# Kernel optimization log

Measured on AMD Instinct MI355X. Metric: run time of the kernel, lower is better.

## Reference

```python
import jax, jax.numpy as jnp
import numpy as np

SIGMA = 1.2
SIGMA_SQ = jnp.float32(SIGMA * SIGMA)


def setup_inputs() -> dict:
    key = jax.random.key(0)
    k1, k2, k3 = jax.random.split(key, 3)
    X = jax.random.normal(k1, (32768, 2), dtype=jnp.float32)
    pattern_layer = jax.random.normal(k2, (8192, 2), dtype=jnp.float32)
    W2 = jax.random.normal(k3, (8192,), dtype=jnp.float32)
    return {"X": X, "pattern_layer": pattern_layer, "W2": W2}


def reference(X, pattern_layer, W2):
    # Pairwise squared distances via |a|^2 + |b|^2 - 2 a.b  -> [N, P]
    x_sq = jnp.sum(X * X, axis=1, keepdims=True)              # [N, 1]
    p_sq = jnp.sum(pattern_layer * pattern_layer, axis=1)     # [P]
    cross = X @ pattern_layer.T                               # [N, P]
    Dsq = x_sq + p_sq[None, :] - 2.0 * cross                  # [N, P]
    K = jnp.exp(-Dsq / (2.0 * SIGMA_SQ))                      # RBF kernel [N, P]
    num = K @ W2                                              # [N]
    den = jnp.sum(K, axis=1)                                  # [N]
    return num / den
```

## Files before the change

kernel.cpp:

```cpp
#include <hip/hip_runtime.h>

#define N 32768
#define P 8192
#define SLICES 16
#define XPB 64
#define PATS_PER_SLICE (P / SLICES)
#define PAIRS_PER_SLICE (PATS_PER_SLICE / 2)

#define RBF_F 0.50093577808645257f

typedef float v2f __attribute__((ext_vector_type(2)));

static __device__ __forceinline__ float fast_exp2(float x) {
#if __has_builtin(__builtin_amdgcn_exp2f)
    return __builtin_amdgcn_exp2f(x);
#else
    return exp2f(x);
#endif
}

__global__ void prep_kernel(const float* __restrict__ pat,
                            const float* __restrict__ w2,
                            float4* __restrict__ c) {
    int q = blockIdx.x * blockDim.x + threadIdx.x;
    if (q < P / 2) {
        float p00 = pat[4 * q + 0], p01 = pat[4 * q + 1];
        float p10 = pat[4 * q + 2], p11 = pat[4 * q + 3];
        float4 a, b;
        a.x = 2.0f * RBF_F * p00;  a.y = 2.0f * RBF_F * p10;
        a.z = 2.0f * RBF_F * p01;  a.w = 2.0f * RBF_F * p11;
        b.x = -RBF_F * (p00 * p00 + p01 * p01);
        b.y = -RBF_F * (p10 * p10 + p11 * p11);
        b.z = w2[2 * q];           b.w = w2[2 * q + 1];
        c[2 * q]     = a;
        c[2 * q + 1] = b;
    }
}

__global__ __launch_bounds__(SLICES * XPB) void
rbf_kernel(const float* __restrict__ X,
           const float4* __restrict__ c,
           float* __restrict__ out) {
    const int t  = threadIdx.x;
    const int xl = t & (XPB - 1);
    const int xi = blockIdx.x * XPB + xl;
    const int slice = __builtin_amdgcn_readfirstlane(t >> 6);

    const float2 xv = ((const float2*)X)[xi];
    const v2f x0v = { xv.x, xv.x };
    const v2f x1v = { xv.y, xv.y };

    const float4* __restrict__ cp = c + (size_t)slice * (2 * PAIRS_PER_SLICE);

    v2f n0 = {0.f, 0.f}, n1 = {0.f, 0.f};
    v2f d0 = {0.f, 0.f}, d1 = {0.f, 0.f};

#pragma unroll 2
    for (int q = 0; q < PAIRS_PER_SLICE; q += 2) {
        float4 a0 = cp[2 * q + 0];
        float4 a1 = cp[2 * q + 1];
        float4 b0 = cp[2 * q + 2];
        float4 b1 = cp[2 * q + 3];

        v2f ta = __builtin_elementwise_fma((v2f){a0.x, a0.y}, x0v,
                                           (v2f){a1.x, a1.y});
        ta = __builtin_elementwise_fma((v2f){a0.z, a0.w}, x1v, ta);
        v2f tb = __builtin_elementwise_fma((v2f){b0.x, b0.y}, x0v,
                                           (v2f){b1.x, b1.y});
        tb = __builtin_elementwise_fma((v2f){b0.z, b0.w}, x1v, tb);

        v2f ka = { fast_exp2(ta.x), fast_exp2(ta.y) };
        v2f kb = { fast_exp2(tb.x), fast_exp2(tb.y) };

        d0 += ka;
        n0 = __builtin_elementwise_fma(ka, (v2f){a1.z, a1.w}, n0);
        d1 += kb;
        n1 = __builtin_elementwise_fma(kb, (v2f){b1.z, b1.w}, n1);
    }

    v2f nv = n0 + n1;
    v2f dv = d0 + d1;
    float num = nv.x + nv.y;
    float den = dv.x + dv.y;

    __shared__ float snum[SLICES][XPB];
    __shared__ float sden[SLICES][XPB];
    snum[slice][xl] = num;
    sden[slice][xl] = den;
    __syncthreads();

    if (t < XPB) {
        float nn = 0.f, dd = 0.f;
#pragma unroll
        for (int s = 0; s < SLICES; ++s) {
            nn += snum[s][t];
            dd += sden[s][t];
        }
        out[blockIdx.x * XPB + t] = nn / dd;
    }
}

extern "C" void kernel_launch(void* const* d_in, const int* in_sizes, int n_in,
                              void* d_out, int out_size, void* d_ws, size_t ws_size,
                              hipStream_t stream) {
    const float* X   = (const float*)d_in[0];
    const float* pat = (const float*)d_in[1];
    const float* w2  = (const float*)d_in[2];
    float* out = (float*)d_out;
    float4* c = (float4*)d_ws;

    prep_kernel<<<(P / 2 + 255) / 256, 256, 0, stream>>>(pat, w2, c);
    rbf_kernel<<<N / XPB, SLICES * XPB, 0, stream>>>(X, c, out);
}
```

Measured before the change: 99.15 us.

## Register-tile multiple X points per lane with lane-distributed patterns and shuffle reduction

Restructures the RBF kernel so each lane handles distinct pattern pairs while keeping eight X points in registers, reusing every loaded pattern coefficient across those points. The pattern loads are software-prefetched one iteration ahead, and per-point partial sums are reduced with wave shuffles before a small shared-memory combine. This targets the per-element load traffic of the previous one-point-per-lane scheme, at the cost of more registers and a reduction epilogue.

```diff
diff --git a/kernel.cpp b/kernel.cpp
--- a/kernel.cpp
+++ b/kernel.cpp
@@ -2,10 +2,15 @@
 
 #define N 32768
 #define P 8192
-#define SLICES 16
-#define XPB 64
-#define PATS_PER_SLICE (P / SLICES)
-#define PAIRS_PER_SLICE (PATS_PER_SLICE / 2)
+#define MX 8
+#define XG 2
+#define PH 2
+#define THREADS (XG * PH * 64)
+#define XPB (XG * MX)
+#define NBLK (N / XPB)
+#define PAIRS (P / 2)
+#define PAIRS_PER_PH (PAIRS / PH)
+#define ITERS (PAIRS_PER_PH / 64)
 
 #define RBF_F 0.50093577808645257f
 
@@ -37,65 +42,85 @@
     }
 }
 
-__global__ __launch_bounds__(SLICES * XPB) void
+__global__ __launch_bounds__(THREADS) void
 rbf_kernel(const float* __restrict__ X,
            const float4* __restrict__ c,
            float* __restrict__ out) {
-    const int t  = threadIdx.x;
-    const int xl = t & (XPB - 1);
-    const int xi = blockIdx.x * XPB + xl;
-    const int slice = __builtin_amdgcn_readfirstlane(t >> 6);
+    const int t    = threadIdx.x;
+    const int lane = t & 63;
+    const int w    = __builtin_amdgcn_readfirstlane(t >> 6);
+    const int xg   = w >> 1;
+    const int ph   = w & 1;
 
-    const float2 xv = ((const float2*)X)[xi];
-    const v2f x0v = { xv.x, xv.x };
-    const v2f x1v = { xv.y, xv.y };
-
-    const float4* __restrict__ cp = c + (size_t)slice * (2 * PAIRS_PER_SLICE);
-
-    v2f n0 = {0.f, 0.f}, n1 = {0.f, 0.f};
-    v2f d0 = {0.f, 0.f}, d1 = {0.f, 0.f};
-
-#pragma unroll 2
-    for (int q = 0; q < PAIRS_PER_SLICE; q += 2) {
-        float4 a0 = cp[2 * q + 0];
-        float4 a1 = cp[2 * q + 1];
-        float4 b0 = cp[2 * q + 2];
-        float4 b1 = cp[2 * q + 3];
-
-        v2f ta = __builtin_elementwise_fma((v2f){a0.x, a0.y}, x0v,
-                                           (v2f){a1.x, a1.y});
-        ta = __builtin_elementwise_fma((v2f){a0.z, a0.w}, x1v, ta);
-        v2f tb = __builtin_elementwise_fma((v2f){b0.x, b0.y}, x0v,
-                                           (v2f){b1.x, b1.y});
-        tb = __builtin_elementwise_fma((v2f){b0.z, b0.w}, x1v, tb);
-
-        v2f ka = { fast_exp2(ta.x), fast_exp2(ta.y) };
-        v2f kb = { fast_exp2(tb.x), fast_exp2(tb.y) };
-
-        d0 += ka;
-        n0 = __builtin_elementwise_fma(ka, (v2f){a1.z, a1.w}, n0);
-        d1 += kb;
-        n1 = __builtin_elementwise_fma(kb, (v2f){b1.z, b1.w}, n1);
+    const int xb = blockIdx.x * XPB + xg * MX;
+    const float2* Xp = (const float2*)X;
+    v2f xs0[MX], xs1[MX];
+#pragma unroll
+    for (int i = 0; i < MX; ++i) {
+        float2 xv = Xp[xb + i];
+        xs0[i] = (v2f){xv.x, xv.x};
+        xs1[i] = (v2f){xv.y, xv.y};
     }
 
-    v2f nv = n0 + n1;
-    v2f dv = d0 + d1;
-    float num = nv.x + nv.y;
-    float den = dv.x + dv.y;
+    v2f num2[MX], den2[MX];
+#pragma unroll
+    for (int i = 0; i < MX; ++i) {
+        num2[i] = (v2f){0.f, 0.f};
+        den2[i] = (v2f){0.f, 0.f};
+    }
 
-    __shared__ float snum[SLICES][XPB];
-    __shared__ float sden[SLICES][XPB];
-    snum[slice][xl] = num;
-    sden[slice][xl] = den;
+    const float4* __restrict__ C4 = c + (size_t)ph * (2 * PAIRS_PER_PH);
+
+    float4 a = C4[2 * lane];
+    float4 b = C4[2 * lane + 1];
+
+    for (int j = 0; j < ITERS; ++j) {
+        const int qn = (((j + 1) & (ITERS - 1)) << 6) + lane;
+        float4 an = C4[2 * qn];
+        float4 bn = C4[2 * qn + 1];
+
+#pragma unroll
+        for (int i = 0; i < MX; ++i) {
+            v2f tt = __builtin_elementwise_fma((v2f){a.x, a.y}, xs0[i],
+                                               (v2f){b.x, b.y});
+            tt = __builtin_elementwise_fma((v2f){a.z, a.w}, xs1[i], tt);
+            v2f k = (v2f){fast_exp2(tt.x), fast_exp2(tt.y)};
+            den2[i] += k;
+            num2[i] = __builtin_elementwise_fma(k, (v2f){b.z, b.w}, num2[i]);
+        }
+        a = an;
+        b = bn;
+    }
+
+    float num[MX], den[MX];
+#pragma unroll
+    for (int i = 0; i < MX; ++i) {
+        num[i] = num2[i].x + num2[i].y;
+        den[i] = den2[i].x + den2[i].y;
+    }
+#pragma unroll
+    for (int m = 1; m < 64; m <<= 1) {
+#pragma unroll
+        for (int i = 0; i < MX; ++i) {
+            num[i] += __shfl_xor(num[i], m, 64);
+            den[i] += __shfl_xor(den[i], m, 64);
+        }
+    }
+
+    __shared__ float red[XG][PH][MX][2];
+    if (lane == 0) {
+#pragma unroll
+        for (int i = 0; i < MX; ++i) {
+            red[xg][ph][i][0] = num[i];
+            red[xg][ph][i][1] = den[i];
+        }
+    }
     __syncthreads();
 
     if (t < XPB) {
-        float nn = 0.f, dd = 0.f;
-#pragma unroll
-        for (int s = 0; s < SLICES; ++s) {
-            nn += snum[s][t];
-            dd += sden[s][t];
-        }
+        int g = t >> 3, xi = t & 7;
+        float nn = red[g][0][xi][0] + red[g][1][xi][0];
+        float dd = red[g][0][xi][1] + red[g][1][xi][1];
         out[blockIdx.x * XPB + t] = nn / dd;
     }
 }
@@ -110,5 +135,5 @@
     float4* c = (float4*)d_ws;
 
     prep_kernel<<<(P / 2 + 255) / 256, 256, 0, stream>>>(pat, w2, c);
-    rbf_kernel<<<N / XPB, SLICES * XPB, 0, stream>>>(X, c, out);
+    rbf_kernel<<<NBLK, THREADS, 0, stream>>>(X, c, out);
 }
```

Measured after the change: 94.43 us. 4.8% less time.
